# Optimization experiments

Measured on AMD Instinct MI355X. Metric: run time of the kernel, lower is better.

Reference implementation:

```python
import jax, jax.numpy as jnp
import numpy as np

B, T, D = 2, 1024, 1024
H, DH = 16, 64          # d_head = d_model // n_heads
MAX_POS = 64


def setup_inputs() -> dict:
    key = jax.random.key(0)
    ks = jax.random.split(key, 11)
    s = 1.0 / np.sqrt(D)
    x = jax.random.normal(ks[0], (B, T, D), jnp.float32)
    Wq = jax.random.normal(ks[1], (D, D), jnp.float32) * s
    Wk = jax.random.normal(ks[2], (D, D), jnp.float32) * s
    Wv = jax.random.normal(ks[3], (D, D), jnp.float32) * s
    Wo = jax.random.normal(ks[4], (D, D), jnp.float32) * s
    bq = jnp.zeros((D,), jnp.float32)
    bk = jnp.zeros((D,), jnp.float32)
    bv = jnp.zeros((D,), jnp.float32)
    bo = jnp.zeros((D,), jnp.float32)
    pos_emb = jax.random.normal(ks[5], (H, MAX_POS, DH), jnp.float32) * 0.02
    causal_mask = jnp.triu(jnp.ones((T, T), bool), k=1)  # True = masked (j > i)
    return dict(x=x, Wq=Wq, bq=bq, Wk=Wk, bk=bk, Wv=Wv, bv=bv, Wo=Wo, bo=bo,
                pos_emb=pos_emb, causal_mask=causal_mask)


def reference(x, Wq, bq, Wk, bk, Wv, bv, Wo, bo, pos_emb, causal_mask):
    Bv, Tv, _ = x.shape
    scale = np.sqrt(DH).astype(np.float32)

    def proj(W, b):
        return (x @ W.T + b).reshape(Bv, Tv, H, DH).transpose(0, 2, 1, 3)  # (B,H,T,d)

    Q, K, V = proj(Wq, bq), proj(Wk, bk), proj(Wv, bv)

    qk = jnp.einsum('bhid,bhjd->bhij', Q, K)              # (B,H,T,T)
    gates = jax.nn.sigmoid(qk / scale)
    gates = jnp.where(causal_mask, 0.0, gates)
    cum = jnp.cumsum(gates, axis=-1)
    pos = cum[..., -1:] - cum                             # total - cumsum_left

    pos = jnp.clip(pos, 0.0, MAX_POS - 1.0)
    pos_floor = jnp.floor(pos)
    alpha = (pos - pos_floor)[..., None]                  # (B,H,T,T,1) -> broadcast
    fidx = pos_floor.astype(jnp.int32)
    cidx = jnp.clip(jnp.ceil(pos), 0, MAX_POS - 1).astype(jnp.int32)

    # q_i . PE_{i,j} via precomputed q.pos_emb table (same math, no (B,H,T,T,d) tensor)
    qpe_tab = jnp.einsum('bhid,hpd->bhip', Q, pos_emb)    # (B,H,T,MAX_POS)
    qpe_f = jnp.take_along_axis(qpe_tab, fidx, axis=-1)   # (B,H,T,T)
    qpe_c = jnp.take_along_axis(qpe_tab, cidx, axis=-1)
    q_pe = (1.0 - alpha[..., 0]) * qpe_f + alpha[..., 0] * qpe_c

    scores = (qk + q_pe) / scale
    scores = jnp.where(causal_mask, -jnp.inf, scores)
    attn = jax.nn.softmax(scores, axis=-1)

    out = jnp.einsum('bhij,bhjd->bhid', attn, V)
    out = out.transpose(0, 2, 1, 3).reshape(Bv, Tv, D)
    return out @ Wo.T + bo
```

## Files before the change

### kernel.cpp

```cpp
#include <hip/hip_runtime.h>
#include <math.h>

#define Tt 1024
#define Dd 1024
#define Hh 16
#define DHh 64
#define MAXPOS 64
#define BTt 2048

typedef short short8 __attribute__((ext_vector_type(8)));
typedef float floatx4 __attribute__((ext_vector_type(4)));

#define MFMA16 __builtin_amdgcn_mfma_f32_16x16x32_bf16

__device__ __forceinline__ unsigned short f2bf(float f) {
    unsigned u;
    __builtin_memcpy(&u, &f, 4);
    u = (u + 0x7FFFu + ((u >> 16) & 1u)) >> 16;
    return (unsigned short)u;
}
__device__ __forceinline__ float bf2fs(short s) {
    unsigned u = ((unsigned)(unsigned short)s) << 16;
    float f;
    __builtin_memcpy(&f, &u, 4);
    return f;
}
__device__ __forceinline__ float fsigm(float x) {
    return __builtin_amdgcn_rcpf(1.f + __expf(-x));
}

__global__ __launch_bounds__(256) void conv_bf16(
    const float* __restrict__ x,  const float* __restrict__ W0,
    const float* __restrict__ W1, const float* __restrict__ W2,
    const float* __restrict__ W3,
    short* __restrict__ xb, short* __restrict__ w0b, short* __restrict__ w1b,
    short* __restrict__ w2b, short* __restrict__ w3b)
{
    const float* src; short* dst; int n;
    switch (blockIdx.y) {
        case 0:  src = x;  dst = xb;  n = BTt * Dd; break;
        case 1:  src = W0; dst = w0b; n = Dd * Dd;  break;
        case 2:  src = W1; dst = w1b; n = Dd * Dd;  break;
        case 3:  src = W2; dst = w2b; n = Dd * Dd;  break;
        default: src = W3; dst = w3b; n = Dd * Dd;  break;
    }
    int idx = (blockIdx.x * 256 + threadIdx.x) * 8;
    if (idx >= n) return;
    floatx4 a0 = *(const floatx4*)&src[idx];
    floatx4 a1 = *(const floatx4*)&src[idx + 4];
    short8 s;
    for (int e = 0; e < 4; ++e) {
        s[e]     = (short)f2bf(a0[e]);
        s[e + 4] = (short)f2bf(a1[e]);
    }
    *(short8*)&dst[idx] = s;
}

#define BM 128
#define BN 128
#define BKK 64
#define LDSS 72

template <int MODE>
__device__ __forceinline__ void gemm_body(const short* __restrict__ A,
                                          const short* __restrict__ W,
                                          const float* __restrict__ bias,
                                          void* __restrict__ Cout,
                                          int N, int K)
{
    __shared__ __align__(16) short Ash[BM * LDSS];
    __shared__ __align__(16) short Bsh[BN * LDSS];
    const int t = threadIdx.x;
    const int lane = t & 63, wave = t >> 6;
    const int wm = wave >> 1, wn = wave & 1;
    const int quad = lane >> 4, l16 = lane & 15;
    const int row0 = blockIdx.x * BM, col0 = blockIdx.y * BN;

    floatx4 acc[4][4];
    for (int a = 0; a < 4; ++a)
        for (int b2 = 0; b2 < 4; ++b2)
            acc[a][b2] = (floatx4){0.f, 0.f, 0.f, 0.f};

    for (int kb = 0; kb < K; kb += BKK) {
        __syncthreads();
        for (int q2 = 0; q2 < 4; ++q2) {
            int ch = t + 256 * q2;
            int r = ch >> 3, c = ch & 7;
            *(short8*)&Ash[r * LDSS + c * 8] =
                *(const short8*)&A[(size_t)(row0 + r) * K + kb + c * 8];
            *(short8*)&Bsh[r * LDSS + c * 8] =
                *(const short8*)&W[(size_t)(col0 + r) * K + kb + c * 8];
        }
        __syncthreads();
        for (int ks = 0; ks < BKK / 32; ++ks) {
            short8 af[4], bfr[4];
            for (int tm = 0; tm < 4; ++tm)
                af[tm] = *(short8*)&Ash[(wm * 64 + tm * 16 + l16) * LDSS + ks * 32 + quad * 8];
            for (int tn = 0; tn < 4; ++tn)
                bfr[tn] = *(short8*)&Bsh[(wn * 64 + tn * 16 + l16) * LDSS + ks * 32 + quad * 8];
            for (int tm = 0; tm < 4; ++tm)
                for (int tn = 0; tn < 4; ++tn)
                    acc[tm][tn] = MFMA16(af[tm], bfr[tn], acc[tm][tn], 0, 0, 0);
        }
    }
    for (int tm = 0; tm < 4; ++tm)
        for (int tn = 0; tn < 4; ++tn) {
            int col = col0 + wn * 64 + tn * 16 + l16;
            float bv = bias[col];
            for (int r = 0; r < 4; ++r) {
                int row = row0 + wm * 64 + tm * 16 + quad * 4 + r;
                float v = acc[tm][tn][r] + bv;
                if (MODE == 0) ((float*)Cout)[(size_t)row * N + col] = v;
                else           ((short*)Cout)[(size_t)row * N + col] = (short)f2bf(v);
            }
        }
}

__global__ __launch_bounds__(256) void gemm_qkv(
    const short* __restrict__ xb,
    const short* __restrict__ Wqb, const short* __restrict__ Wkb,
    const short* __restrict__ Wvb,
    const float* __restrict__ bq, const float* __restrict__ bk,
    const float* __restrict__ bv,
    short* __restrict__ Qb, short* __restrict__ Kb, short* __restrict__ Vrow)
{
    if (blockIdx.z == 0)      gemm_body<1>(xb, Wqb, bq, Qb, Dd, Dd);
    else if (blockIdx.z == 1) gemm_body<1>(xb, Wkb, bk, Kb, Dd, Dd);
    else                      gemm_body<1>(xb, Wvb, bv, Vrow, Dd, Dd);
}

__global__ __launch_bounds__(256) void gemm_o(
    const short* __restrict__ A, const short* __restrict__ W,
    const float* __restrict__ bias, float* __restrict__ C)
{
    gemm_body<0>(A, W, bias, C, Dd, Dd);
}

__global__ __launch_bounds__(256) void v_transpose(
    const short* __restrict__ Vrow, short* __restrict__ Vt)
{
    __shared__ __align__(16) short L[64 * 72];
    const int t = threadIdx.x;
    const int j0 = blockIdx.x * 64, d0 = blockIdx.y * 64, b = blockIdx.z;
    for (int s = 0; s < 2; ++s) {
        int c = t * 2 + s;
        int jr = c >> 3, c8 = c & 7;
        *(short8*)&L[jr * 72 + c8 * 8] =
            *(const short8*)&Vrow[((size_t)(b * Tt + j0 + jr)) * Dd + d0 + c8 * 8];
    }
    __syncthreads();
    for (int s = 0; s < 2; ++s) {
        int c = t * 2 + s;
        int dr = c >> 3, c8 = c & 7;
        short8 v;
        for (int e = 0; e < 8; ++e) v[e] = L[(c8 * 8 + e) * 72 + dr];
        *(short8*)&Vt[((size_t)(b * Dd + d0 + dr)) * Tt + j0 + c8 * 8] = v;
    }
}

__global__ __launch_bounds__(256) void cope_attn(
    const short* __restrict__ Q, const short* __restrict__ K,
    const short* __restrict__ Vt, const float* __restrict__ PE,
    short* __restrict__ AOb)
{
    const int h = blockIdx.y, b = blockIdx.z;
    const int t = threadIdx.x, lane = t & 63, wave = t >> 6;
    const int quad = lane >> 4, l16 = lane & 15;

    __shared__ __align__(16) short SldS[32 * 264];
    __shared__ __align__(16) short KV[128 * 72];
    __shared__ short qpeB[32 * 68];
    __shared__ float lrow[32];
    float* Sld = (float*)SldS;

    const float inv_scale = 0.125f;
    const int sr = t >> 3, ss = t & 7;

    for (int phase = 0; phase < 2; ++phase) {
        const int it = (phase == 0) ? (31 - (int)blockIdx.x) : (int)blockIdx.x;
        const int i0 = it * 32;
        const int irow = i0 + sr;

        short* QtS = SldS;
        {
            int r = t >> 3, c = t & 7;
            *(short8*)&QtS[r * 72 + c * 8] =
                *(const short8*)&Q[((size_t)(b * Tt + i0 + r)) * Dd + h * DHh + c * 8];
        }
        for (int e = 0; e < 16; ++e) {
            int idx = t + 256 * e;
            int p = idx >> 6, d = idx & 63;
            KV[p * 72 + d] = (short)f2bf(PE[((size_t)h * MAXPOS + p) * DHh + d]);
        }
        __syncthreads();

        short8 qa[2][2];
        for (int rb = 0; rb < 2; ++rb)
            for (int ks = 0; ks < 2; ++ks)
                qa[rb][ks] = *(short8*)&QtS[(rb * 16 + l16) * 72 + ks * 32 + quad * 8];

        {
            int mt = wave >> 1;
            int ntA = 2 * (wave & 1), ntB = ntA + 1;
            floatx4 c0f = {0, 0, 0, 0}, c1f = {0, 0, 0, 0};
            for (int ks = 0; ks < 2; ++ks) {
                short8 b0 = *(short8*)&KV[(ntA * 16 + l16) * 72 + ks * 32 + quad * 8];
                short8 b1 = *(short8*)&KV[(ntB * 16 + l16) * 72 + ks * 32 + quad * 8];
                c0f = MFMA16(qa[mt][ks], b0, c0f, 0, 0, 0);
                c1f = MFMA16(qa[mt][ks], b1, c1f, 0, 0, 0);
            }
            for (int r = 0; r < 4; ++r) {
                qpeB[(mt * 16 + quad * 4 + r) * 68 + ntA * 16 + l16] = (short)f2bf(c0f[r]);
                qpeB[(mt * 16 + quad * 4 + r) * 68 + ntB * 16 + l16] = (short)f2bf(c1f[r]);
            }
        }

        const int JT = (i0 + 159) >> 7;
        floatx4 o0 = {0, 0, 0, 0}, o1 = {0, 0, 0, 0};
        const int pv_mt = wave >> 1;
        const int pv_ntA = 2 * (wave & 1), pv_ntB = pv_ntA + 1;
        float l_acc = 0.f;
        float rightAcc = 0.f;

        short8 kreg[4];
        for (int e = 0; e < 4; ++e) {
            int ch = t + 256 * e;
            int jr = ch >> 3, c = ch & 7;
            kreg[e] = *(const short8*)&K[((size_t)(b * Tt + (JT - 1) * 128 + jr)) * Dd + h * DHh + c * 8];
        }

        for (int jt = JT - 1; jt >= 0; --jt) {
            const int j0 = jt * 128;
            __syncthreads();
            for (int e = 0; e < 4; ++e) {
                int ch = t + 256 * e;
                int jr = ch >> 3, c = ch & 7;
                *(short8*)&KV[jr * 72 + c * 8] = kreg[e];
            }
            __syncthreads();
            {
                int ntA = 2 * wave, ntB = ntA + 1;
                floatx4 c00 = {0,0,0,0}, c01 = {0,0,0,0}, c10 = {0,0,0,0}, c11 = {0,0,0,0};
                for (int ks = 0; ks < 2; ++ks) {
                    short8 b0 = *(short8*)&KV[(ntA * 16 + l16) * 72 + ks * 32 + quad * 8];
                    short8 b1 = *(short8*)&KV[(ntB * 16 + l16) * 72 + ks * 32 + quad * 8];
                    c00 = MFMA16(qa[0][ks], b0, c00, 0, 0, 0);
                    c01 = MFMA16(qa[0][ks], b1, c01, 0, 0, 0);
                    c10 = MFMA16(qa[1][ks], b0, c10, 0, 0, 0);
                    c11 = MFMA16(qa[1][ks], b1, c11, 0, 0, 0);
                }
                for (int r = 0; r < 4; ++r) {
                    Sld[(quad * 4 + r) * 132 + ntA * 16 + l16] = c00[r];
                    Sld[(quad * 4 + r) * 132 + ntB * 16 + l16] = c01[r];
                    Sld[(16 + quad * 4 + r) * 132 + ntA * 16 + l16] = c10[r];
                    Sld[(16 + quad * 4 + r) * 132 + ntB * 16 + l16] = c11[r];
                }
            }
            __syncthreads();
            short8 vreg[4];
            for (int e = 0; e < 4; ++e) {
                int ch = t + 256 * e;
                int d = ch >> 4, c = ch & 15;
                vreg[e] = *(const short8*)&Vt[((size_t)(b * Dd + h * DHh + d)) * Tt + j0 + c * 8];
            }
            if (jt > 0) {
                for (int e = 0; e < 4; ++e) {
                    int ch = t + 256 * e;
                    int jr = ch >> 3, c = ch & 7;
                    kreg[e] = *(const short8*)&K[((size_t)(b * Tt + j0 - 128 + jr)) * Dd + h * DHh + c * 8];
                }
            }
            {
                floatx4 qv[4];
                for (int q4 = 0; q4 < 4; ++q4) {
                    short8 qraw = *(short8*)&SldS[sr * 264 + ss * 32 + q4 * 8];
                    __builtin_memcpy(&qv[q4], &qraw, 16);
                }
                float gt[16];
                float gs = 0.f;
                for (int e = 0; e < 16; ++e) {
                    int j = j0 + ss * 16 + e;
                    float qk = qv[e >> 2][e & 3];
                    float g = (j <= irow) ? fsigm(qk * inv_scale) : 0.f;
                    gt[e] = g;
                    gs += g;
                }
                float inc = gs;
                for (int d2 = 1; d2 < 8; d2 <<= 1) {
                    float n = __shfl_down(inc, d2, 64);
                    if ((lane & 7) + d2 < 8) inc += n;
                }
                float tileTot = __shfl(inc, lane & 56, 64);
                float base = rightAcc + (inc - gs);
                float run = 0.f;
                short8 p0, p1;
                for (int e = 15; e >= 0; --e) {
                    int j = j0 + ss * 16 + e;
                    float pos = base + run;
                    run += gt[e];
                    pos = fminf(fmaxf(pos, 0.f), 63.f);
                    float pf = floorf(pos);
                    float al = pos - pf;
                    int fi = (int)pf;
                    int ci = fi + 1; if (ci > 63) ci = 63;
                    float qp = (1.f - al) * bf2fs(qpeB[sr * 68 + fi]) + al * bf2fs(qpeB[sr * 68 + ci]);
                    float qk = qv[e >> 2][e & 3];
                    float p = (j <= irow) ? __expf((qk + qp) * inv_scale) : 0.f;
                    if (e < 8) p0[e] = (short)f2bf(p); else p1[e - 8] = (short)f2bf(p);
                    l_acc += p;
                }
                *(short8*)&SldS[sr * 264 + ss * 32]     = p0;
                *(short8*)&SldS[sr * 264 + ss * 32 + 8] = p1;
                rightAcc += tileTot;
            }
            for (int e = 0; e < 4; ++e) {
                int ch = t + 256 * e;
                int d = ch >> 4, c = ch & 15;
                *(short8*)&KV[d * 136 + c * 8] = vreg[e];
            }
            __syncthreads();
            for (int ks = 0; ks < 4; ++ks) {
                short8 a  = *(short8*)&SldS[(pv_mt * 16 + l16) * 264 + ks * 64
                                            + ((quad >> 1) << 5) + ((quad & 1) << 3)];
                short8 b0 = *(short8*)&KV[(pv_ntA * 16 + l16) * 136 + ks * 32 + quad * 8];
                short8 b1 = *(short8*)&KV[(pv_ntB * 16 + l16) * 136 + ks * 32 + quad * 8];
                o0 = MFMA16(a, b0, o0, 0, 0, 0);
                o1 = MFMA16(a, b1, o1, 0, 0, 0);
            }
        }
        float lr = l_acc;
        for (int d2 = 4; d2 >= 1; d2 >>= 1) lr += __shfl_xor(lr, d2, 64);
        if (ss == 0) lrow[sr] = lr;
        __syncthreads();
        for (int r = 0; r < 4; ++r) {
            int row = pv_mt * 16 + quad * 4 + r;
            float inv = __builtin_amdgcn_rcpf(lrow[row]);
            size_t off = ((size_t)(b * Tt + i0 + row)) * Dd + h * DHh;
            AOb[off + pv_ntA * 16 + l16] = (short)f2bf(o0[r] * inv);
            AOb[off + pv_ntB * 16 + l16] = (short)f2bf(o1[r] * inv);
        }
    }
}

extern "C" void kernel_launch(void* const* d_in, const int* in_sizes, int n_in,
                              void* d_out, int out_size, void* d_ws, size_t ws_size,
                              hipStream_t stream)
{
    const float* x  = (const float*)d_in[0];
    const float* Wq = (const float*)d_in[1];
    const float* bq = (const float*)d_in[2];
    const float* Wk = (const float*)d_in[3];
    const float* bk = (const float*)d_in[4];
    const float* Wv = (const float*)d_in[5];
    const float* bv = (const float*)d_in[6];
    const float* Wo = (const float*)d_in[7];
    const float* bo = (const float*)d_in[8];
    const float* pe = (const float*)d_in[9];

    short* xb   = (short*)d_ws;
    short* Wqb  = xb   + (size_t)BTt * Dd;
    short* Wkb  = Wqb  + (size_t)Dd * Dd;
    short* Wvb  = Wkb  + (size_t)Dd * Dd;
    short* Wob  = Wvb  + (size_t)Dd * Dd;
    short* Qb   = Wob  + (size_t)Dd * Dd;
    short* Kb   = Qb   + (size_t)BTt * Dd;
    short* Vrow = Kb   + (size_t)BTt * Dd;
    short* Vtg  = Vrow + (size_t)BTt * Dd;
    short* AOb  = Vtg  + (size_t)BTt * Dd;

    dim3 gc(BTt * Dd / 8 / 256, 5);
    conv_bf16<<<gc, 256, 0, stream>>>(x, Wq, Wk, Wv, Wo, xb, Wqb, Wkb, Wvb, Wob);

    dim3 gq(BTt / BM, Dd / BN, 3);
    gemm_qkv<<<gq, 256, 0, stream>>>(xb, Wqb, Wkb, Wvb, bq, bk, bv, Qb, Kb, Vrow);

    dim3 gv(Tt / 64, Dd / 64, 2);
    v_transpose<<<gv, 256, 0, stream>>>(Vrow, Vtg);

    dim3 ga(Tt / 32 / 2, Hh, 2);
    cope_attn<<<ga, 256, 0, stream>>>(Qb, Kb, Vtg, pe, AOb);

    dim3 go(BTt / BM, Dd / BN, 1);
    gemm_o<<<go, 256, 0, stream>>>(AOb, Wob, bo, (float*)d_out);
}
```

Measured before the change: 182.3 us.

## Load GEMM tiles via direct global-to-LDS loads and shrink N tile to 64

The shared GEMM body now moves A and W tiles into LDS with global_load_lds instead of staging them through registers. It also changes the block tile from 128x128 to 128x64, with each wave owning 32 rows, and drops the padded LDS stride. The aim is to cut register pressure and VGPR staging traffic and to double the number of blocks for the QKV and output projections. In exchange, the unpadded 64-short stride may cause LDS bank conflicts on fragment reads, and B-tile reuse per block is lower.

```diff
diff --git a/kernel.cpp b/kernel.cpp
--- a/kernel.cpp
+++ b/kernel.cpp
@@ -27,6 +27,12 @@
 }
 __device__ __forceinline__ float fsigm(float x) {
     return __builtin_amdgcn_rcpf(1.f + __expf(-x));
+}
+__device__ __forceinline__ void gl2lds16(const short* __restrict__ g, short* l) {
+    __builtin_amdgcn_global_load_lds(
+        (const __attribute__((address_space(1))) void*)g,
+        (__attribute__((address_space(3))) void*)l,
+        16, 0, 0);
 }
 
 __global__ __launch_bounds__(256) void conv_bf16(
@@ -56,11 +62,6 @@
     *(short8*)&dst[idx] = s;
 }
 
-#define BM 128
-#define BN 128
-#define BKK 64
-#define LDSS 72
-
 template <int MODE>
 __device__ __forceinline__ void gemm_body(const short* __restrict__ A,
                                           const short* __restrict__ W,
@@ -68,47 +69,50 @@
                                           void* __restrict__ Cout,
                                           int N, int K)
 {
-    __shared__ __align__(16) short Ash[BM * LDSS];
-    __shared__ __align__(16) short Bsh[BN * LDSS];
+    __shared__ __align__(16) short Ash[128 * 64];
+    __shared__ __align__(16) short Bsh[64 * 64];
     const int t = threadIdx.x;
     const int lane = t & 63, wave = t >> 6;
-    const int wm = wave >> 1, wn = wave & 1;
     const int quad = lane >> 4, l16 = lane & 15;
-    const int row0 = blockIdx.x * BM, col0 = blockIdx.y * BN;
-
-    floatx4 acc[4][4];
-    for (int a = 0; a < 4; ++a)
+    const int row0 = blockIdx.x * 128, col0 = blockIdx.y * 64;
+
+    const int g_r = lane >> 3, g_c = (lane & 7) * 8;
+
+    floatx4 acc[2][4];
+    for (int a = 0; a < 2; ++a)
         for (int b2 = 0; b2 < 4; ++b2)
             acc[a][b2] = (floatx4){0.f, 0.f, 0.f, 0.f};
 
-    for (int kb = 0; kb < K; kb += BKK) {
+    for (int kb = 0; kb < K; kb += 64) {
+        if (kb) __syncthreads();
+        for (int i = 0; i < 4; ++i) {
+            int rbase = (wave * 4 + i) * 8;
+            gl2lds16(&A[(size_t)(row0 + rbase + g_r) * K + kb + g_c],
+                     &Ash[rbase * 64]);
+        }
+        for (int i = 0; i < 2; ++i) {
+            int rbase = (wave * 2 + i) * 8;
+            gl2lds16(&W[(size_t)(col0 + rbase + g_r) * K + kb + g_c],
+                     &Bsh[rbase * 64]);
+        }
         __syncthreads();
-        for (int q2 = 0; q2 < 4; ++q2) {
-            int ch = t + 256 * q2;
-            int r = ch >> 3, c = ch & 7;
-            *(short8*)&Ash[r * LDSS + c * 8] =
-                *(const short8*)&A[(size_t)(row0 + r) * K + kb + c * 8];
-            *(short8*)&Bsh[r * LDSS + c * 8] =
-                *(const short8*)&W[(size_t)(col0 + r) * K + kb + c * 8];
-        }
-        __syncthreads();
-        for (int ks = 0; ks < BKK / 32; ++ks) {
-            short8 af[4], bfr[4];
-            for (int tm = 0; tm < 4; ++tm)
-                af[tm] = *(short8*)&Ash[(wm * 64 + tm * 16 + l16) * LDSS + ks * 32 + quad * 8];
+        for (int ks = 0; ks < 2; ++ks) {
+            short8 af[2], bfr[4];
+            for (int tm = 0; tm < 2; ++tm)
+                af[tm] = *(short8*)&Ash[(wave * 32 + tm * 16 + l16) * 64 + ks * 32 + quad * 8];
             for (int tn = 0; tn < 4; ++tn)
-                bfr[tn] = *(short8*)&Bsh[(wn * 64 + tn * 16 + l16) * LDSS + ks * 32 + quad * 8];
-            for (int tm = 0; tm < 4; ++tm)
+                bfr[tn] = *(short8*)&Bsh[(tn * 16 + l16) * 64 + ks * 32 + quad * 8];
+            for (int tm = 0; tm < 2; ++tm)
                 for (int tn = 0; tn < 4; ++tn)
                     acc[tm][tn] = MFMA16(af[tm], bfr[tn], acc[tm][tn], 0, 0, 0);
         }
     }
-    for (int tm = 0; tm < 4; ++tm)
+    for (int tm = 0; tm < 2; ++tm)
         for (int tn = 0; tn < 4; ++tn) {
-            int col = col0 + wn * 64 + tn * 16 + l16;
+            int col = col0 + tn * 16 + l16;
             float bv = bias[col];
             for (int r = 0; r < 4; ++r) {
-                int row = row0 + wm * 64 + tm * 16 + quad * 4 + r;
+                int row = row0 + wave * 32 + tm * 16 + quad * 4 + r;
                 float v = acc[tm][tn][r] + bv;
                 if (MODE == 0) ((float*)Cout)[(size_t)row * N + col] = v;
                 else           ((short*)Cout)[(size_t)row * N + col] = (short)f2bf(v);
@@ -371,7 +375,7 @@
     dim3 gc(BTt * Dd / 8 / 256, 5);
     conv_bf16<<<gc, 256, 0, stream>>>(x, Wq, Wk, Wv, Wo, xb, Wqb, Wkb, Wvb, Wob);
 
-    dim3 gq(BTt / BM, Dd / BN, 3);
+    dim3 gq(BTt / 128, Dd / 64, 3);
     gemm_qkv<<<gq, 256, 0, stream>>>(xb, Wqb, Wkb, Wvb, bq, bk, bv, Qb, Kb, Vrow);
 
     dim3 gv(Tt / 64, Dd / 64, 2);
@@ -380,6 +384,6 @@
     dim3 ga(Tt / 32 / 2, Hh, 2);
     cope_attn<<<ga, 256, 0, stream>>>(Qb, Kb, Vtg, pe, AOb);
 
-    dim3 go(BTt / BM, Dd / BN, 1);
+    dim3 go(BTt / 128, Dd / 64, 1);
     gemm_o<<<go, 256, 0, stream>>>(AOb, Wob, bo, (float*)d_out);
 }
```

After: 181.0 us. About the same (-0.7%).
